# Optimization experiments

Hardware: AMD Instinct MI355X
Metric: run time of the kernel (lower is better)

The kernel has to match this reference:

```python
import jax, jax.numpy as jnp
import numpy as np

B = 8192       # atmospheric columns (batch)
NLAY = 60      # vertical levels (RNN sequence length)
NX = 4         # per-level input features
NXS = 3        # surface scalar inputs
NH1 = 64       # rnn1 hidden
NH2 = 64       # rnn2 hidden
NMEM = 16      # latent memory width (nh_mem)
NY = 4         # per-level outputs
NYS = 3        # surface outputs


def _lstm(x, h0, c0, Wih, Whh, bih, bhh):
    """PyTorch-convention LSTM (gate order i,f,g,o). x: [B,T,nx] -> ([B,T,nh], hL, cL)."""
    b = bih + bhh
    WihT = Wih.T
    WhhT = Whh.T

    def step(carry, xt):
        h, c = carry
        g = xt @ WihT + h @ WhhT + b
        i, f, gg, o = jnp.split(g, 4, axis=-1)
        c = jax.nn.sigmoid(f) * c + jax.nn.sigmoid(i) * jnp.tanh(gg)
        h = jax.nn.sigmoid(o) * jnp.tanh(c)
        return (h, c), h

    (hL, cL), ys = jax.lax.scan(step, (h0, c0), jnp.swapaxes(x, 0, 1))
    return jnp.swapaxes(ys, 0, 1), hL, cL


def setup_inputs() -> dict:
    key = jax.random.key(0)
    ks = jax.random.split(key, 30)

    def p(i, shape):
        return jax.random.normal(ks[i], shape, jnp.float32) * 0.05

    return {
        "inputs_main": jax.random.normal(ks[0], (B, NLAY, NX), jnp.float32),
        "inputs_aux": jax.random.normal(ks[1], (B, NXS), jnp.float32),
        "rnn1_mem": jax.random.normal(ks[2], (B, NLAY, NMEM), jnp.float32),
        # mlp_initial: Linear(nx, nneur[0])
        "Wi": p(3, (NH1, NX)), "bi": p(4, (NH1,)),
        # mlp_surface1/2: Linear(nx_sfc, nh_rnn1)
        "Ws1": p(5, (NH1, NXS)), "bs1": p(6, (NH1,)),
        "Ws2": p(7, (NH1, NXS)), "bs2": p(8, (NH1,)),
        # mlp_toa1/2: Linear(1, nh_rnn2)
        "Wt1": p(9, (NH2, 1)), "bt1": p(10, (NH2,)),
        "Wt2": p(11, (NH2, 1)), "bt2": p(12, (NH2,)),
        # rnn1: LSTM(NH1+NMEM -> NH1)
        "Wih1": p(13, (4 * NH1, NH1 + NMEM)), "Whh1": p(14, (4 * NH1, NH1)),
        "bih1": p(15, (4 * NH1,)), "bhh1": p(16, (4 * NH1,)),
        # rnn2: LSTM(NH1 -> NH2)
        "Wih2": p(17, (4 * NH2, NH1)), "Whh2": p(18, (4 * NH2, NH2)),
        "bih2": p(19, (4 * NH2,)), "bhh2": p(20, (4 * NH2,)),
        # mlp_latent: Linear(NH2, NMEM)
        "Wl": p(21, (NMEM, NH2)), "bl": p(22, (NMEM,)),
        # mlp_output: Linear(NMEM, NY)
        "Wo": p(23, (NY, NMEM)), "bo": p(24, (NY,)),
        # mlp_surface_output: Linear(NH2, NYS)
        "Wso": p(25, (NYS, NH2)), "bso": p(26, (NYS,)),
    }


def reference(inputs_main, inputs_aux, rnn1_mem, Wi, bi, Ws1, bs1, Ws2, bs2,
              Wt1, bt1, Wt2, bt2, Wih1, Whh1, bih1, bhh1, Wih2, Whh2, bih2, bhh2,
              Wl, bl, Wo, bo, Wso, bso):
    # initial MLP + tanh
    x = jnp.tanh(inputs_main @ Wi.T + bi)                       # [B,L,NH1]
    # concat convective memory
    x = jnp.concatenate([x, rnn1_mem], axis=2)                  # [B,L,NH1+NMEM]
    # rnn1 runs surface->TOA: flip level axis
    x = jnp.flip(x, axis=1)
    hx = jnp.tanh(inputs_aux @ Ws1.T + bs1)                     # surface-conditioned h0
    cx = jnp.tanh(inputs_aux @ Ws2.T + bs2)
    r1, _, _ = _lstm(x, hx, cx, Wih1, Whh1, bih1, bhh1)
    r1 = jnp.flip(r1, axis=1)                                   # back to TOA->surface
    # rnn2 initialized from TOA scalar
    toa = inputs_aux[:, 1:2]
    hx2 = toa @ Wt1.T + bt1
    cx2 = toa @ Wt2.T + bt2
    r2, hL, _ = _lstm(r1, hx2, cx2, Wih2, Whh2, bih2, bhh2)     # [B,L,NH2]
    # intermediate latent MLP -> new per-level memory
    lat = r2 @ Wl.T + bl                                        # [B,L,NMEM]
    new_mem = lat
    out = lat @ Wo.T + bo                                       # [B,L,NY]
    out_sfc = hL @ Wso.T + bso                                  # [B,NYS]
    return (out, out_sfc, new_mem)
```

## Files before the change

### kernel.cpp

```cpp
#include <hip/hip_runtime.h>
#include <hip/hip_bf16.h>

#define BATCH 8192
#define NLAY  60
#define ROWS  16
#define TPB   256
#define SX    136
#define SM    968
#define SI    244
#define LOG2E 1.44269504089f
#define T2L   2.88539008178f

typedef unsigned short ushort_t;
typedef __attribute__((ext_vector_type(8))) short short8;
typedef __attribute__((ext_vector_type(4))) float f32x4;
typedef __attribute__((ext_vector_type(4))) float f4v;

__device__ __forceinline__ float rcp_(float x) { return __builtin_amdgcn_rcpf(x); }
__device__ __forceinline__ float ex2_(float x) { return __builtin_amdgcn_exp2f(x); }
__device__ __forceinline__ ushort_t f2bu(float f) {
  unsigned u = __float_as_uint(f);
  return (ushort_t)((u + 0x7FFFu + ((u >> 16) & 1u)) >> 16);
}
__device__ __forceinline__ unsigned pkbf(float a, float b) {
  union { __hip_bfloat162 h; unsigned u; } c;
  c.h = __float22bfloat162_rn(make_float2(a, b));
  return c.u;
}
__device__ __forceinline__ f32x4 mfma16(short8 a, short8 b, f32x4 c) {
  return __builtin_amdgcn_mfma_f32_16x16x32_bf16(a, b, c, 0, 0, 0);
}
#define BAR() asm volatile("s_waitcnt lgkmcnt(0)\n\ts_barrier" ::: "memory")

__global__ void wtranspose(const float* __restrict__ Wih1, const float* __restrict__ Whh1,
                           const float* __restrict__ Wih2, const float* __restrict__ Whh2,
                           const float* __restrict__ Wl,   const float* __restrict__ Wo,
                           const float* __restrict__ Wso,  ushort_t* __restrict__ frag) {
  int e = blockIdx.x * 256 + threadIdx.x;
  float v;
  if (e < 40960) {
    int j = e & 7, lx = (e >> 3) & 63, rest = e >> 9;
    int ks = rest % 5, gw = rest / 5;
    int g = gw & 3, wv = gw >> 2;
    int row = g * 64 + wv * 16 + (lx & 15);
    int k = ks * 32 + (lx >> 4) * 8 + j;
    v = (k < 64)  ? Wih1[row * 80 + k]
      : (k < 128) ? Whh1[row * 64 + (k - 64)]
      : (k < 144) ? Wih1[row * 80 + 64 + (k - 128)]
      : 0.0f;
    v *= (g == 2) ? T2L : LOG2E;
  } else if (e < 73728) {
    int e2 = e - 40960;
    int j = e2 & 7, lx = (e2 >> 3) & 63, rest = e2 >> 9;
    int ks = rest & 3, g = (rest >> 2) & 3, wv = rest >> 4;
    int row = g * 64 + wv * 16 + (lx & 15);
    int k = ks * 32 + (lx >> 4) * 8 + j;
    v = (k < 64) ? Wih2[row * 64 + k] : Whh2[row * 64 + (k - 64)];
    v *= (g == 2) ? T2L : LOG2E;
  } else if (e < 74752) {
    int e3 = e - 73728;
    int j = e3 & 7, lx = (e3 >> 3) & 63, ks = e3 >> 9;
    int n = lx & 15, k = ks * 32 + (lx >> 4) * 8 + j;
    v = Wl[n * 64 + k];
  } else if (e < 75776) {
    int e4 = e - 74752;
    int j = e4 & 7, lx = (e4 >> 3) & 63, ks = e4 >> 9;
    int n = lx & 15, k = ks * 32 + (lx >> 4) * 8 + j;
    v = 0.0f;
    if (n < 4) {
#pragma unroll
      for (int m = 0; m < 16; ++m) v += Wo[n * 16 + m] * Wl[m * 64 + k];
    }
  } else {
    int e5 = e - 75776;
    int j = e5 & 7, lx = (e5 >> 3) & 63, ks = e5 >> 9;
    int n = lx & 15, k = ks * 32 + (lx >> 4) * 8 + j;
    v = (n < 3) ? Wso[n * 64 + k] : 0.0f;
  }
  frag[e] = f2bu(v);
}

__global__ __launch_bounds__(TPB, 2)
void lstm_fused(const float* __restrict__ inputs_main, const float* __restrict__ inputs_aux,
                const float* __restrict__ rnn1_mem,
                const float* __restrict__ Wi,  const float* __restrict__ bi,
                const float* __restrict__ Ws1, const float* __restrict__ bs1,
                const float* __restrict__ Ws2, const float* __restrict__ bs2,
                const float* __restrict__ Wt1, const float* __restrict__ bt1,
                const float* __restrict__ Wt2, const float* __restrict__ bt2,
                const float* __restrict__ bih1, const float* __restrict__ bhh1,
                const float* __restrict__ bih2, const float* __restrict__ bhh2,
                const float* __restrict__ bl,  const float* __restrict__ Wo,
                const float* __restrict__ bo,  const float* __restrict__ bso,
                const ushort_t* __restrict__ frag,
                ushort_t* __restrict__ r1buf,
                float* __restrict__ out, float* __restrict__ out_sfc,
                float* __restrict__ new_mem) {
  const ushort_t* W1f = frag;
  const ushort_t* W2f = frag + 40960;
  const ushort_t* WlF = frag + 73728;
  const ushort_t* WcF = frag + 74752;
  const ushort_t* WsF = frag + 75776;

  __shared__ __align__(16) ushort_t xh[2][16 * SX];
  __shared__ __align__(16) ushort_t memAll[16 * SM];
  __shared__ __align__(16) float    inm[16 * SI];

  const int tid = threadIdx.x;
  const int lane = tid & 63, w = tid >> 6;
  const int ln = lane & 15, lq = lane >> 4;
  const int u = w * 16 + ln;
  const int rowbase = lq * 4;
  const int b0 = blockIdx.x * ROWS;
  const int xr = tid >> 4, xm = tid & 15, xc0 = xm * 4;
  const int rr8 = tid >> 3, ch8 = tid & 7;

  ushort_t* r1blk = r1buf + (size_t)blockIdx.x * (60 * 16 * 64);

  short8 B1f[4][5];
#pragma unroll
  for (int g = 0; g < 4; ++g)
#pragma unroll
    for (int ks = 0; ks < 5; ++ks)
      B1f[g][ks] = *(const short8*)(W1f + (((w * 4 + g) * 5 + ks) << 9) + (lane << 3));
  float bg1[4];
#pragma unroll
  for (int g = 0; g < 4; ++g)
    bg1[g] = (bih1[g * 64 + u] + bhh1[g * 64 + u]) * ((g == 2) ? T2L : LOG2E);

  f4v wif[4];
#pragma unroll
  for (int cc = 0; cc < 4; ++cc) wif[cc] = *(const f4v*)(Wi + (xc0 + cc) * 4) * T2L;
  f4v bifv = *(const f4v*)(bi + xc0) * T2L;

  for (int e = tid; e < 16 * 240; e += TPB) {
    int r = e / 240, c = e - r * 240;
    inm[r * SI + c] = inputs_main[(size_t)(b0 + r) * 240 + c];
  }
  for (int e = tid; e < 16 * 960; e += TPB) {
    int r = e / 960, c = e - r * 960;
    memAll[r * SM + c] = f2bu(rnn1_mem[(size_t)(b0 + r) * 960 + c]);
  }
  __syncthreads();

  float ct1[4];
  {
    f4v xin = *(const f4v*)&inm[xr * SI + 59 * 4];
    float xp[4];
#pragma unroll
    for (int cc = 0; cc < 4; ++cc) {
      float a = fmaf(wif[cc][3], xin[3], fmaf(wif[cc][2], xin[2],
                fmaf(wif[cc][1], xin[1], fmaf(wif[cc][0], xin[0], bifv[cc]))));
      xp[cc] = fmaf(rcp_(1.0f + ex2_(a)), -2.0f, 1.0f);
    }
    *(uint2*)&xh[0][xr * SX + xc0] = make_uint2(pkbf(xp[0], xp[1]), pkbf(xp[2], xp[3]));

    float w10 = Ws1[u * 3 + 0] * T2L, w11 = Ws1[u * 3 + 1] * T2L, w12 = Ws1[u * 3 + 2] * T2L;
    float bb1 = bs1[u] * T2L;
    float w20 = Ws2[u * 3 + 0] * T2L, w21 = Ws2[u * 3 + 1] * T2L, w22 = Ws2[u * 3 + 2] * T2L;
    float bb2 = bs2[u] * T2L;
#pragma unroll
    for (int reg = 0; reg < 4; ++reg) {
      int row = rowbase + reg;
      const float* ax = inputs_aux + (size_t)(b0 + row) * 3;
      float a0 = ax[0], a1 = ax[1], a2 = ax[2];
      float ha = w10 * a0 + w11 * a1 + w12 * a2 + bb1;
      xh[0][row * SX + 64 + u] = f2bu(fmaf(rcp_(1.0f + ex2_(ha)), -2.0f, 1.0f));
      float ca = w20 * a0 + w21 * a1 + w22 * a2 + bb2;
      ct1[reg] = fmaf(rcp_(1.0f + ex2_(ca)), -2.0f * T2L, T2L);
    }
  }
  __syncthreads();

  ushort_t* r1t = r1blk + rowbase * 64 + u;
  unsigned sxv[4], syv[4];
  int pb = 0;

  for (int tg = 14; tg >= 0; --tg) {
#pragma unroll
    for (int s = 3; s >= 0; --s) {
      const int t = tg * 4 + s;
      const int nb = pb ^ 1;
      const ushort_t* xrow = &xh[pb][ln * SX];
      short8 af0 = *(const short8*)(xrow + lq * 8);
      short8 af1 = *(const short8*)(xrow + 32 + lq * 8);
      short8 af2 = *(const short8*)(xrow + 64 + lq * 8);
      short8 af3 = *(const short8*)(xrow + 96 + lq * 8);
      short8 af4 = {};
      if (lq < 2) af4 = *(const short8*)(memAll + ln * SM + t * 16 + lq * 8);

      f32x4 acc[4];
#pragma unroll
      for (int g = 0; g < 4; ++g) acc[g] = (f32x4){bg1[g], bg1[g], bg1[g], bg1[g]};
      __builtin_amdgcn_s_setprio(1);
#pragma unroll
      for (int g = 0; g < 4; ++g) {
        acc[g] = mfma16(af0, B1f[g][0], acc[g]);
        acc[g] = mfma16(af1, B1f[g][1], acc[g]);
        acc[g] = mfma16(af2, B1f[g][2], acc[g]);
        acc[g] = mfma16(af3, B1f[g][3], acc[g]);
        acc[g] = mfma16(af4, B1f[g][4], acc[g]);
      }
      __builtin_amdgcn_s_setprio(0);

      if (t > 0) {
        f4v xin = *(const f4v*)&inm[xr * SI + (t - 1) * 4];
        float xp[4];
#pragma unroll
        for (int cc = 0; cc < 4; ++cc) {
          float a = fmaf(wif[cc][3], xin[3], fmaf(wif[cc][2], xin[2],
                    fmaf(wif[cc][1], xin[1], fmaf(wif[cc][0], xin[0], bifv[cc]))));
          xp[cc] = fmaf(rcp_(1.0f + ex2_(a)), -2.0f, 1.0f);
        }
        *(uint2*)&xh[nb][xr * SX + xc0] = make_uint2(pkbf(xp[0], xp[1]), pkbf(xp[2], xp[3]));
      }

      float h[4];
#pragma unroll
      for (int reg = 0; reg < 4; ++reg) {
        float si = rcp_(1.0f + ex2_(-acc[0][reg]));
        float sf = rcp_(1.0f + ex2_(-acc[1][reg]));
        float so = rcp_(1.0f + ex2_(-acc[3][reg]));
        float gt = fmaf(rcp_(1.0f + ex2_(acc[2][reg])), -2.0f * T2L, T2L);
        ct1[reg] = fmaf(sf, ct1[reg], si * gt);
        float tc = fmaf(rcp_(1.0f + ex2_(ct1[reg])), -2.0f, 1.0f);
        h[reg] = so * tc;
      }
      unsigned h01 = pkbf(h[0], h[1]), h23 = pkbf(h[2], h[3]);
      sxv[s] = h01; syv[s] = h23;
      if (t > 0) {
        xh[nb][(rowbase + 0) * SX + 64 + u] = (ushort_t)h01;
        xh[nb][(rowbase + 1) * SX + 64 + u] = (ushort_t)(h01 >> 16);
        xh[nb][(rowbase + 2) * SX + 64 + u] = (ushort_t)h23;
        xh[nb][(rowbase + 3) * SX + 64 + u] = (ushort_t)(h23 >> 16);
      } else {
        xh[nb][(rowbase + 0) * SX + u] = (ushort_t)h01;
        xh[nb][(rowbase + 1) * SX + u] = (ushort_t)(h01 >> 16);
        xh[nb][(rowbase + 2) * SX + u] = (ushort_t)h23;
        xh[nb][(rowbase + 3) * SX + u] = (ushort_t)(h23 >> 16);
      }
      BAR();
      pb = nb;
    }
    ushort_t* rp = r1t + (tg << 12);
#pragma unroll
    for (int s = 0; s < 4; ++s) {
      unsigned a = sxv[s], b = syv[s];
      rp[s * 1024 + 0 * 64] = (ushort_t)a;
      rp[s * 1024 + 1 * 64] = (ushort_t)(a >> 16);
      rp[s * 1024 + 2 * 64] = (ushort_t)b;
      rp[s * 1024 + 3 * 64] = (ushort_t)(b >> 16);
    }
  }

  short8 B2f[4][4];
#pragma unroll
  for (int g = 0; g < 4; ++g)
#pragma unroll
    for (int ks = 0; ks < 4; ++ks)
      B2f[g][ks] = *(const short8*)(W2f + (((w * 4 + g) * 4 + ks) << 9) + (lane << 3));
  float bg2[4];
#pragma unroll
  for (int g = 0; g < 4; ++g)
    bg2[g] = (bih2[g * 64 + u] + bhh2[g * 64 + u]) * ((g == 2) ? T2L : LOG2E);

  float ct2[4];
  {
    float wt1u = Wt1[u], wt2u = Wt2[u], bt1u = bt1[u], bt2u = bt2[u];
#pragma unroll
    for (int reg = 0; reg < 4; ++reg) {
      int row = rowbase + reg;
      float toa = inputs_aux[(size_t)(b0 + row) * 3 + 1];
      xh[pb][row * SX + 64 + u] = f2bu(toa * wt1u + bt1u);
      ct2[reg] = (toa * wt2u + bt2u) * T2L;
    }
  }
  short8 PW0 = {}, PW1 = {};
  float pbias = 0.0f;
  if (w == 0) {
    PW0 = *(const short8*)(WlF + (lane << 3));
    PW1 = *(const short8*)(WlF + 512 + (lane << 3));
    pbias = bl[ln];
  } else if (w == 1) {
    PW0 = *(const short8*)(WcF + (lane << 3));
    PW1 = *(const short8*)(WcF + 512 + (lane << 3));
    if (ln < 4) {
      float a = bo[ln];
#pragma unroll
      for (int m = 0; m < 16; ++m) a += Wo[ln * 16 + m] * bl[m];
      pbias = a;
    }
  } else if (w == 2) {
    PW0 = *(const short8*)(WsF + (lane << 3));
    PW1 = *(const short8*)(WsF + 512 + (lane << 3));
    pbias = (ln < 3) ? bso[ln] : 0.0f;
  }
  const ushort_t* r1rp = r1blk + 1024 + rr8 * 64 + ch8 * 8;
  float* nmb = new_mem + (size_t)(b0 + rowbase) * 960 + ln;
  float* outb = out + (size_t)(b0 + rowbase) * 240 + ln;
  f32x4 pst[4];
  __syncthreads();

  for (int tg = 0; tg < 15; ++tg) {
#pragma unroll
    for (int s = 0; s < 4; ++s) {
      const int t = tg * 4 + s;
      const int nb = pb ^ 1;
      short8 r1v = {};
      if (t < 59 && tid < 128) r1v = *(const short8*)(r1rp + t * 1024);

      const ushort_t* xrow = &xh[pb][ln * SX];
      short8 af0 = *(const short8*)(xrow + lq * 8);
      short8 af1 = *(const short8*)(xrow + 32 + lq * 8);
      short8 af2 = *(const short8*)(xrow + 64 + lq * 8);
      short8 af3 = *(const short8*)(xrow + 96 + lq * 8);

      f32x4 acc[4];
#pragma unroll
      for (int g = 0; g < 4; ++g) acc[g] = (f32x4){bg2[g], bg2[g], bg2[g], bg2[g]};
      __builtin_amdgcn_s_setprio(1);
#pragma unroll
      for (int g = 0; g < 4; ++g) {
        acc[g] = mfma16(af0, B2f[g][0], acc[g]);
        acc[g] = mfma16(af1, B2f[g][1], acc[g]);
        acc[g] = mfma16(af2, B2f[g][2], acc[g]);
        acc[g] = mfma16(af3, B2f[g][3], acc[g]);
      }

      if (t > 0 && w < 2) {
        f32x4 ap = (f32x4){pbias, pbias, pbias, pbias};
        ap = mfma16(af2, PW0, ap);
        ap = mfma16(af3, PW1, ap);
        pst[(t - 1) & 3] = ap;
      }
      __builtin_amdgcn_s_setprio(0);

      float h[4];
#pragma unroll
      for (int reg = 0; reg < 4; ++reg) {
        float si = rcp_(1.0f + ex2_(-acc[0][reg]));
        float sf = rcp_(1.0f + ex2_(-acc[1][reg]));
        float so = rcp_(1.0f + ex2_(-acc[3][reg]));
        float gt = fmaf(rcp_(1.0f + ex2_(acc[2][reg])), -2.0f * T2L, T2L);
        ct2[reg] = fmaf(sf, ct2[reg], si * gt);
        float tc = fmaf(rcp_(1.0f + ex2_(ct2[reg])), -2.0f, 1.0f);
        h[reg] = so * tc;
      }
      unsigned h01 = pkbf(h[0], h[1]), h23 = pkbf(h[2], h[3]);
      xh[nb][(rowbase + 0) * SX + 64 + u] = (ushort_t)h01;
      xh[nb][(rowbase + 1) * SX + 64 + u] = (ushort_t)(h01 >> 16);
      xh[nb][(rowbase + 2) * SX + 64 + u] = (ushort_t)h23;
      xh[nb][(rowbase + 3) * SX + 64 + u] = (ushort_t)(h23 >> 16);
      if (t < 59 && tid < 128)
        *(short8*)&xh[nb][rr8 * SX + ch8 * 8] = r1v;
      BAR();
      pb = nb;
    }
    if (w < 2) {
      const int base = tg * 4;
#pragma unroll
      for (int k = 0; k < 4; ++k) {
        const int pt = (k == 3) ? base - 1 : base + k;
        if (pt < 0) continue;
        f32x4 ap = pst[k];
        if (w == 0) {
#pragma unroll
          for (int reg = 0; reg < 4; ++reg) nmb[reg * 960 + pt * 16] = ap[reg];
        } else if (ln < 4) {
#pragma unroll
          for (int reg = 0; reg < 4; ++reg) outb[reg * 240 + pt * 4] = ap[reg];
        }
      }
    }
  }

  if (w < 3) {
    const ushort_t* xrow = &xh[pb][ln * SX];
    short8 aL0 = *(const short8*)(xrow + 64 + lq * 8);
    short8 aL1 = *(const short8*)(xrow + 96 + lq * 8);
    f32x4 ap = (f32x4){pbias, pbias, pbias, pbias};
    ap = mfma16(aL0, PW0, ap);
    ap = mfma16(aL1, PW1, ap);
    if (w == 0) {
#pragma unroll
      for (int reg = 0; reg < 4; ++reg) nmb[reg * 960 + 59 * 16] = ap[reg];
    } else if (w == 1) {
      if (ln < 4) {
#pragma unroll
        for (int reg = 0; reg < 4; ++reg) outb[reg * 240 + 59 * 4] = ap[reg];
      }
    } else {
      if (ln < 3) {
#pragma unroll
        for (int reg = 0; reg < 4; ++reg)
          out_sfc[(size_t)(b0 + rowbase + reg) * 3 + ln] = ap[reg];
      }
    }
  }
}

extern "C" void kernel_launch(void* const* d_in, const int* in_sizes, int n_in,
                              void* d_out, int out_size, void* d_ws, size_t ws_size,
                              hipStream_t stream) {
  (void)in_sizes; (void)n_in; (void)out_size; (void)ws_size;
  const float* inputs_main = (const float*)d_in[0];
  const float* inputs_aux  = (const float*)d_in[1];
  const float* rnn1_mem    = (const float*)d_in[2];
  const float* Wi   = (const float*)d_in[3];
  const float* bi   = (const float*)d_in[4];
  const float* Ws1  = (const float*)d_in[5];
  const float* bs1  = (const float*)d_in[6];
  const float* Ws2  = (const float*)d_in[7];
  const float* bs2  = (const float*)d_in[8];
  const float* Wt1  = (const float*)d_in[9];
  const float* bt1  = (const float*)d_in[10];
  const float* Wt2  = (const float*)d_in[11];
  const float* bt2  = (const float*)d_in[12];
  const float* Wih1 = (const float*)d_in[13];
  const float* Whh1 = (const float*)d_in[14];
  const float* bih1 = (const float*)d_in[15];
  const float* bhh1 = (const float*)d_in[16];
  const float* Wih2 = (const float*)d_in[17];
  const float* Whh2 = (const float*)d_in[18];
  const float* bih2 = (const float*)d_in[19];
  const float* bhh2 = (const float*)d_in[20];
  const float* Wl   = (const float*)d_in[21];
  const float* bl   = (const float*)d_in[22];
  const float* Wo   = (const float*)d_in[23];
  const float* bo   = (const float*)d_in[24];
  const float* Wso  = (const float*)d_in[25];
  const float* bso  = (const float*)d_in[26];

  float* out     = (float*)d_out;
  float* out_sfc = out + (size_t)BATCH * NLAY * 4;
  float* new_mem = out_sfc + (size_t)BATCH * 3;

  ushort_t* frag  = (ushort_t*)d_ws;
  ushort_t* r1buf = (ushort_t*)((char*)d_ws + 153600);

  wtranspose<<<300, 256, 0, stream>>>(Wih1, Whh1, Wih2, Whh2, Wl, Wo, Wso, frag);
  lstm_fused<<<BATCH / ROWS, TPB, 0, stream>>>(
      inputs_main, inputs_aux, rnn1_mem, Wi, bi, Ws1, bs1, Ws2, bs2,
      Wt1, bt1, Wt2, bt2, bih1, bhh1, bih2, bhh2, bl, Wo, bo, bso,
      frag, r1buf, out, out_sfc, new_mem);
}
```

Before: 253.9 us.

## Process two 16-row groups per block to interleave independent LSTM recurrences

Each block now handles 32 batch rows as two independent 16-row groups, issuing both groups' MFMA chains and gate math in each timestep. Two independent dependency chains per wave are meant to hide MFMA and transcendental latency within the serial recurrence, and one barrier now covers both groups. In exchange the grid halves to 256 blocks, launch bounds drop to one block per SIMD set, and LDS and register use roughly double. That cuts the number of resident waves and may leave some CUs idle.

Result: slower. 293.4 us (+15.5%).

```diff
diff --git a/kernel.cpp b/kernel.cpp
--- a/kernel.cpp
+++ b/kernel.cpp
@@ -3,7 +3,7 @@
 
 #define BATCH 8192
 #define NLAY  60
-#define ROWS  16
+#define ROWS  32
 #define TPB   256
 #define SX    136
 #define SM    968
@@ -80,7 +80,7 @@
   frag[e] = f2bu(v);
 }
 
-__global__ __launch_bounds__(TPB, 2)
+__global__ __launch_bounds__(TPB, 1)
 void lstm_fused(const float* __restrict__ inputs_main, const float* __restrict__ inputs_aux,
                 const float* __restrict__ rnn1_mem,
                 const float* __restrict__ Wi,  const float* __restrict__ bi,
@@ -102,9 +102,9 @@
   const ushort_t* WcF = frag + 74752;
   const ushort_t* WsF = frag + 75776;
 
-  __shared__ __align__(16) ushort_t xh[2][16 * SX];
-  __shared__ __align__(16) ushort_t memAll[16 * SM];
-  __shared__ __align__(16) float    inm[16 * SI];
+  __shared__ __align__(16) ushort_t xh[2][2][16 * SX];
+  __shared__ __align__(16) ushort_t memAll[2][16 * SM];
+  __shared__ __align__(16) float    inm[2][16 * SI];
 
   const int tid = threadIdx.x;
   const int lane = tid & 63, w = tid >> 6;
@@ -112,10 +112,11 @@
   const int u = w * 16 + ln;
   const int rowbase = lq * 4;
   const int b0 = blockIdx.x * ROWS;
-  const int xr = tid >> 4, xm = tid & 15, xc0 = xm * 4;
-  const int rr8 = tid >> 3, ch8 = tid & 7;
-
-  ushort_t* r1blk = r1buf + (size_t)blockIdx.x * (60 * 16 * 64);
+  const int xr = tid >> 4, xc0 = (tid & 15) * 4;
+  const int gsel = tid >> 7, tl = tid & 127;
+  const int rr8 = tl >> 3, ch8 = tl & 7;
+
+  ushort_t* r1blk = r1buf + (size_t)blockIdx.x * (60 * 32 * 64);
 
   short8 B1f[4][5];
 #pragma unroll
@@ -133,47 +134,50 @@
   for (int cc = 0; cc < 4; ++cc) wif[cc] = *(const f4v*)(Wi + (xc0 + cc) * 4) * T2L;
   f4v bifv = *(const f4v*)(bi + xc0) * T2L;
 
-  for (int e = tid; e < 16 * 240; e += TPB) {
+  for (int e = tid; e < 32 * 240; e += TPB) {
     int r = e / 240, c = e - r * 240;
-    inm[r * SI + c] = inputs_main[(size_t)(b0 + r) * 240 + c];
-  }
-  for (int e = tid; e < 16 * 960; e += TPB) {
+    inm[r >> 4][(r & 15) * SI + c] = inputs_main[(size_t)(b0 + r) * 240 + c];
+  }
+  for (int e = tid; e < 32 * 960; e += TPB) {
     int r = e / 960, c = e - r * 960;
-    memAll[r * SM + c] = f2bu(rnn1_mem[(size_t)(b0 + r) * 960 + c]);
+    memAll[r >> 4][(r & 15) * SM + c] = f2bu(rnn1_mem[(size_t)(b0 + r) * 960 + c]);
   }
   __syncthreads();
 
-  float ct1[4];
+  float ct1[2][4];
   {
-    f4v xin = *(const f4v*)&inm[xr * SI + 59 * 4];
-    float xp[4];
-#pragma unroll
-    for (int cc = 0; cc < 4; ++cc) {
-      float a = fmaf(wif[cc][3], xin[3], fmaf(wif[cc][2], xin[2],
-                fmaf(wif[cc][1], xin[1], fmaf(wif[cc][0], xin[0], bifv[cc]))));
-      xp[cc] = fmaf(rcp_(1.0f + ex2_(a)), -2.0f, 1.0f);
-    }
-    *(uint2*)&xh[0][xr * SX + xc0] = make_uint2(pkbf(xp[0], xp[1]), pkbf(xp[2], xp[3]));
-
+#pragma unroll
+    for (int G = 0; G < 2; ++G) {
+      f4v xin = *(const f4v*)&inm[G][xr * SI + 59 * 4];
+      float xp[4];
+#pragma unroll
+      for (int cc = 0; cc < 4; ++cc) {
+        float a = fmaf(wif[cc][3], xin[3], fmaf(wif[cc][2], xin[2],
+                  fmaf(wif[cc][1], xin[1], fmaf(wif[cc][0], xin[0], bifv[cc]))));
+        xp[cc] = fmaf(rcp_(1.0f + ex2_(a)), -2.0f, 1.0f);
+      }
+      *(uint2*)&xh[G][0][xr * SX + xc0] = make_uint2(pkbf(xp[0], xp[1]), pkbf(xp[2], xp[3]));
+    }
     float w10 = Ws1[u * 3 + 0] * T2L, w11 = Ws1[u * 3 + 1] * T2L, w12 = Ws1[u * 3 + 2] * T2L;
     float bb1 = bs1[u] * T2L;
     float w20 = Ws2[u * 3 + 0] * T2L, w21 = Ws2[u * 3 + 1] * T2L, w22 = Ws2[u * 3 + 2] * T2L;
     float bb2 = bs2[u] * T2L;
 #pragma unroll
-    for (int reg = 0; reg < 4; ++reg) {
-      int row = rowbase + reg;
-      const float* ax = inputs_aux + (size_t)(b0 + row) * 3;
-      float a0 = ax[0], a1 = ax[1], a2 = ax[2];
-      float ha = w10 * a0 + w11 * a1 + w12 * a2 + bb1;
-      xh[0][row * SX + 64 + u] = f2bu(fmaf(rcp_(1.0f + ex2_(ha)), -2.0f, 1.0f));
-      float ca = w20 * a0 + w21 * a1 + w22 * a2 + bb2;
-      ct1[reg] = fmaf(rcp_(1.0f + ex2_(ca)), -2.0f * T2L, T2L);
-    }
+    for (int G = 0; G < 2; ++G)
+#pragma unroll
+      for (int reg = 0; reg < 4; ++reg) {
+        int row = rowbase + reg;
+        const float* ax = inputs_aux + (size_t)(b0 + G * 16 + row) * 3;
+        float a0 = ax[0], a1 = ax[1], a2 = ax[2];
+        float ha = w10 * a0 + w11 * a1 + w12 * a2 + bb1;
+        xh[G][0][row * SX + 64 + u] = f2bu(fmaf(rcp_(1.0f + ex2_(ha)), -2.0f, 1.0f));
+        float ca = w20 * a0 + w21 * a1 + w22 * a2 + bb2;
+        ct1[G][reg] = fmaf(rcp_(1.0f + ex2_(ca)), -2.0f * T2L, T2L);
+      }
   }
   __syncthreads();
 
-  ushort_t* r1t = r1blk + rowbase * 64 + u;
-  unsigned sxv[4], syv[4];
+  unsigned sxv[2][4], syv[2][4];
   int pb = 0;
 
   for (int tg = 14; tg >= 0; --tg) {
@@ -181,75 +185,93 @@
     for (int s = 3; s >= 0; --s) {
       const int t = tg * 4 + s;
       const int nb = pb ^ 1;
-      const ushort_t* xrow = &xh[pb][ln * SX];
-      short8 af0 = *(const short8*)(xrow + lq * 8);
-      short8 af1 = *(const short8*)(xrow + 32 + lq * 8);
-      short8 af2 = *(const short8*)(xrow + 64 + lq * 8);
-      short8 af3 = *(const short8*)(xrow + 96 + lq * 8);
-      short8 af4 = {};
-      if (lq < 2) af4 = *(const short8*)(memAll + ln * SM + t * 16 + lq * 8);
-
-      f32x4 acc[4];
-#pragma unroll
-      for (int g = 0; g < 4; ++g) acc[g] = (f32x4){bg1[g], bg1[g], bg1[g], bg1[g]};
+      short8 af[2][5];
+#pragma unroll
+      for (int G = 0; G < 2; ++G) {
+        const ushort_t* xrow = &xh[G][pb][ln * SX];
+        af[G][0] = *(const short8*)(xrow + lq * 8);
+        af[G][1] = *(const short8*)(xrow + 32 + lq * 8);
+        af[G][2] = *(const short8*)(xrow + 64 + lq * 8);
+        af[G][3] = *(const short8*)(xrow + 96 + lq * 8);
+        af[G][4] = (short8){};
+        if (lq < 2) af[G][4] = *(const short8*)(memAll[G] + ln * SM + t * 16 + lq * 8);
+      }
+
+      f32x4 acc[2][4];
+#pragma unroll
+      for (int G = 0; G < 2; ++G)
+#pragma unroll
+        for (int g = 0; g < 4; ++g) acc[G][g] = (f32x4){bg1[g], bg1[g], bg1[g], bg1[g]};
       __builtin_amdgcn_s_setprio(1);
 #pragma unroll
-      for (int g = 0; g < 4; ++g) {
-        acc[g] = mfma16(af0, B1f[g][0], acc[g]);
-        acc[g] = mfma16(af1, B1f[g][1], acc[g]);
-        acc[g] = mfma16(af2, B1f[g][2], acc[g]);
-        acc[g] = mfma16(af3, B1f[g][3], acc[g]);
-        acc[g] = mfma16(af4, B1f[g][4], acc[g]);
-      }
+      for (int g = 0; g < 4; ++g)
+#pragma unroll
+        for (int G = 0; G < 2; ++G) {
+          acc[G][g] = mfma16(af[G][0], B1f[g][0], acc[G][g]);
+          acc[G][g] = mfma16(af[G][1], B1f[g][1], acc[G][g]);
+          acc[G][g] = mfma16(af[G][2], B1f[g][2], acc[G][g]);
+          acc[G][g] = mfma16(af[G][3], B1f[g][3], acc[G][g]);
+          acc[G][g] = mfma16(af[G][4], B1f[g][4], acc[G][g]);
+        }
       __builtin_amdgcn_s_setprio(0);
 
       if (t > 0) {
-        f4v xin = *(const f4v*)&inm[xr * SI + (t - 1) * 4];
-        float xp[4];
-#pragma unroll
-        for (int cc = 0; cc < 4; ++cc) {
-          float a = fmaf(wif[cc][3], xin[3], fmaf(wif[cc][2], xin[2],
-                    fmaf(wif[cc][1], xin[1], fmaf(wif[cc][0], xin[0], bifv[cc]))));
-          xp[cc] = fmaf(rcp_(1.0f + ex2_(a)), -2.0f, 1.0f);
-        }
-        *(uint2*)&xh[nb][xr * SX + xc0] = make_uint2(pkbf(xp[0], xp[1]), pkbf(xp[2], xp[3]));
-      }
-
-      float h[4];
-#pragma unroll
-      for (int reg = 0; reg < 4; ++reg) {
-        float si = rcp_(1.0f + ex2_(-acc[0][reg]));
-        float sf = rcp_(1.0f + ex2_(-acc[1][reg]));
-        float so = rcp_(1.0f + ex2_(-acc[3][reg]));
-        float gt = fmaf(rcp_(1.0f + ex2_(acc[2][reg])), -2.0f * T2L, T2L);
-        ct1[reg] = fmaf(sf, ct1[reg], si * gt);
-        float tc = fmaf(rcp_(1.0f + ex2_(ct1[reg])), -2.0f, 1.0f);
-        h[reg] = so * tc;
-      }
-      unsigned h01 = pkbf(h[0], h[1]), h23 = pkbf(h[2], h[3]);
-      sxv[s] = h01; syv[s] = h23;
-      if (t > 0) {
-        xh[nb][(rowbase + 0) * SX + 64 + u] = (ushort_t)h01;
-        xh[nb][(rowbase + 1) * SX + 64 + u] = (ushort_t)(h01 >> 16);
-        xh[nb][(rowbase + 2) * SX + 64 + u] = (ushort_t)h23;
-        xh[nb][(rowbase + 3) * SX + 64 + u] = (ushort_t)(h23 >> 16);
-      } else {
-        xh[nb][(rowbase + 0) * SX + u] = (ushort_t)h01;
-        xh[nb][(rowbase + 1) * SX + u] = (ushort_t)(h01 >> 16);
-        xh[nb][(rowbase + 2) * SX + u] = (ushort_t)h23;
-        xh[nb][(rowbase + 3) * SX + u] = (ushort_t)(h23 >> 16);
+#pragma unroll
+        for (int G = 0; G < 2; ++G) {
+          f4v xin = *(const f4v*)&inm[G][xr * SI + (t - 1) * 4];
+          float xp[4];
+#pragma unroll
+          for (int cc = 0; cc < 4; ++cc) {
+            float a = fmaf(wif[cc][3], xin[3], fmaf(wif[cc][2], xin[2],
+                      fmaf(wif[cc][1], xin[1], fmaf(wif[cc][0], xin[0], bifv[cc]))));
+            xp[cc] = fmaf(rcp_(1.0f + ex2_(a)), -2.0f, 1.0f);
+          }
+          *(uint2*)&xh[G][nb][xr * SX + xc0] =
+              make_uint2(pkbf(xp[0], xp[1]), pkbf(xp[2], xp[3]));
+        }
+      }
+
+#pragma unroll
+      for (int G = 0; G < 2; ++G) {
+        float h[4];
+#pragma unroll
+        for (int reg = 0; reg < 4; ++reg) {
+          float si = rcp_(1.0f + ex2_(-acc[G][0][reg]));
+          float sf = rcp_(1.0f + ex2_(-acc[G][1][reg]));
+          float so = rcp_(1.0f + ex2_(-acc[G][3][reg]));
+          float gt = fmaf(rcp_(1.0f + ex2_(acc[G][2][reg])), -2.0f * T2L, T2L);
+          ct1[G][reg] = fmaf(sf, ct1[G][reg], si * gt);
+          float tc = fmaf(rcp_(1.0f + ex2_(ct1[G][reg])), -2.0f, 1.0f);
+          h[reg] = so * tc;
+        }
+        unsigned h01 = pkbf(h[0], h[1]), h23 = pkbf(h[2], h[3]);
+        sxv[G][s] = h01; syv[G][s] = h23;
+        if (t > 0) {
+          xh[G][nb][(rowbase + 0) * SX + 64 + u] = (ushort_t)h01;
+          xh[G][nb][(rowbase + 1) * SX + 64 + u] = (ushort_t)(h01 >> 16);
+          xh[G][nb][(rowbase + 2) * SX + 64 + u] = (ushort_t)h23;
+          xh[G][nb][(rowbase + 3) * SX + 64 + u] = (ushort_t)(h23 >> 16);
+        } else {
+          xh[G][nb][(rowbase + 0) * SX + u] = (ushort_t)h01;
+          xh[G][nb][(rowbase + 1) * SX + u] = (ushort_t)(h01 >> 16);
+          xh[G][nb][(rowbase + 2) * SX + u] = (ushort_t)h23;
+          xh[G][nb][(rowbase + 3) * SX + u] = (ushort_t)(h23 >> 16);
+        }
       }
       BAR();
       pb = nb;
     }
-    ushort_t* rp = r1t + (tg << 12);
-#pragma unroll
-    for (int s = 0; s < 4; ++s) {
-      unsigned a = sxv[s], b = syv[s];
-      rp[s * 1024 + 0 * 64] = (ushort_t)a;
-      rp[s * 1024 + 1 * 64] = (ushort_t)(a >> 16);
-      rp[s * 1024 + 2 * 64] = (ushort_t)b;
-      rp[s * 1024 + 3 * 64] = (ushort_t)(b >> 16);
+#pragma unroll
+    for (int G = 0; G < 2; ++G) {
+      ushort_t* rp = r1blk + G * 61440 + (tg << 12) + rowbase * 64 + u;
+#pragma unroll
+      for (int s = 0; s < 4; ++s) {
+        unsigned a = sxv[G][s], b = syv[G][s];
+        rp[s * 1024 + 0 * 64] = (ushort_t)a;
+        rp[s * 1024 + 1 * 64] = (ushort_t)(a >> 16);
+        rp[s * 1024 + 2 * 64] = (ushort_t)b;
+        rp[s * 1024 + 3 * 64] = (ushort_t)(b >> 16);
+      }
     }
   }
 
@@ -264,16 +286,18 @@
   for (int g = 0; g < 4; ++g)
     bg2[g] = (bih2[g * 64 + u] + bhh2[g * 64 + u]) * ((g == 2) ? T2L : LOG2E);
 
-  float ct2[4];
+  float ct2[2][4];
   {
     float wt1u = Wt1[u], wt2u = Wt2[u], bt1u = bt1[u], bt2u = bt2[u];
 #pragma unroll
-    for (int reg = 0; reg < 4; ++reg) {
-      int row = rowbase + reg;
-      float toa = inputs_aux[(size_t)(b0 + row) * 3 + 1];
-      xh[pb][row * SX + 64 + u] = f2bu(toa * wt1u + bt1u);
-      ct2[reg] = (toa * wt2u + bt2u) * T2L;
-    }
+    for (int G = 0; G < 2; ++G)
+#pragma unroll
+      for (int reg = 0; reg < 4; ++reg) {
+        int row = rowbase + reg;
+        float toa = inputs_aux[(size_t)(b0 + G * 16 + row) * 3 + 1];
+        xh[G][pb][row * SX + 64 + u] = f2bu(toa * wt1u + bt1u);
+        ct2[G][reg] = (toa * wt2u + bt2u) * T2L;
+      }
   }
   short8 PW0 = {}, PW1 = {};
   float pbias = 0.0f;
@@ -295,10 +319,14 @@
     PW1 = *(const short8*)(WsF + 512 + (lane << 3));
     pbias = (ln < 3) ? bso[ln] : 0.0f;
   }
-  const ushort_t* r1rp = r1blk + 1024 + rr8 * 64 + ch8 * 8;
-  float* nmb = new_mem + (size_t)(b0 + rowbase) * 960 + ln;
-  float* outb = out + (size_t)(b0 + rowbase) * 240 + ln;
-  f32x4 pst[4];
+  const ushort_t* r1rp = r1blk + gsel * 61440 + 1024 + rr8 * 64 + ch8 * 8;
+  float* nmb[2];  float* outb[2];
+#pragma unroll
+  for (int G = 0; G < 2; ++G) {
+    nmb[G]  = new_mem + (size_t)(b0 + G * 16 + rowbase) * 960 + ln;
+    outb[G] = out + (size_t)(b0 + G * 16 + rowbase) * 240 + ln;
+  }
+  f32x4 pst[2][4];
   __syncthreads();
 
   for (int tg = 0; tg < 15; ++tg) {
@@ -307,93 +335,110 @@
       const int t = tg * 4 + s;
       const int nb = pb ^ 1;
       short8 r1v = {};
-      if (t < 59 && tid < 128) r1v = *(const short8*)(r1rp + t * 1024);
-
-      const ushort_t* xrow = &xh[pb][ln * SX];
-      short8 af0 = *(const short8*)(xrow + lq * 8);
-      short8 af1 = *(const short8*)(xrow + 32 + lq * 8);
-      short8 af2 = *(const short8*)(xrow + 64 + lq * 8);
-      short8 af3 = *(const short8*)(xrow + 96 + lq * 8);
-
-      f32x4 acc[4];
-#pragma unroll
-      for (int g = 0; g < 4; ++g) acc[g] = (f32x4){bg2[g], bg2[g], bg2[g], bg2[g]};
+      if (t < 59) r1v = *(const short8*)(r1rp + t * 1024);
+
+      short8 af[2][4];
+#pragma unroll
+      for (int G = 0; G < 2; ++G) {
+        const ushort_t* xrow = &xh[G][pb][ln * SX];
+        af[G][0] = *(const short8*)(xrow + lq * 8);
+        af[G][1] = *(const short8*)(xrow + 32 + lq * 8);
+        af[G][2] = *(const short8*)(xrow + 64 + lq * 8);
+        af[G][3] = *(const short8*)(xrow + 96 + lq * 8);
+      }
+
+      f32x4 acc[2][4];
+#pragma unroll
+      for (int G = 0; G < 2; ++G)
+#pragma unroll
+        for (int g = 0; g < 4; ++g) acc[G][g] = (f32x4){bg2[g], bg2[g], bg2[g], bg2[g]};
       __builtin_amdgcn_s_setprio(1);
 #pragma unroll
-      for (int g = 0; g < 4; ++g) {
-        acc[g] = mfma16(af0, B2f[g][0], acc[g]);
-        acc[g] = mfma16(af1, B2f[g][1], acc[g]);
-        acc[g] = mfma16(af2, B2f[g][2], acc[g]);
-        acc[g] = mfma16(af3, B2f[g][3], acc[g]);
-      }
-
+      for (int g = 0; g < 4; ++g)
+#pragma unroll
+        for (int G = 0; G < 2; ++G) {
+          acc[G][g] = mfma16(af[G][0], B2f[g][0], acc[G][g]);
+          acc[G][g] = mfma16(af[G][1], B2f[g][1], acc[G][g]);
+          acc[G][g] = mfma16(af[G][2], B2f[g][2], acc[G][g]);
+          acc[G][g] = mfma16(af[G][3], B2f[g][3], acc[G][g]);
+        }
       if (t > 0 && w < 2) {
-        f32x4 ap = (f32x4){pbias, pbias, pbias, pbias};
-        ap = mfma16(af2, PW0, ap);
-        ap = mfma16(af3, PW1, ap);
-        pst[(t - 1) & 3] = ap;
+#pragma unroll
+        for (int G = 0; G < 2; ++G) {
+          f32x4 ap = (f32x4){pbias, pbias, pbias, pbias};
+          ap = mfma16(af[G][2], PW0, ap);
+          ap = mfma16(af[G][3], PW1, ap);
+          pst[G][(t - 1) & 3] = ap;
+        }
       }
       __builtin_amdgcn_s_setprio(0);
 
-      float h[4];
-#pragma unroll
-      for (int reg = 0; reg < 4; ++reg) {
-        float si = rcp_(1.0f + ex2_(-acc[0][reg]));
-        float sf = rcp_(1.0f + ex2_(-acc[1][reg]));
-        float so = rcp_(1.0f + ex2_(-acc[3][reg]));
-        float gt = fmaf(rcp_(1.0f + ex2_(acc[2][reg])), -2.0f * T2L, T2L);
-        ct2[reg] = fmaf(sf, ct2[reg], si * gt);
-        float tc = fmaf(rcp_(1.0f + ex2_(ct2[reg])), -2.0f, 1.0f);
-        h[reg] = so * tc;
-      }
-      unsigned h01 = pkbf(h[0], h[1]), h23 = pkbf(h[2], h[3]);
-      xh[nb][(rowbase + 0) * SX + 64 + u] = (ushort_t)h01;
-      xh[nb][(rowbase + 1) * SX + 64 + u] = (ushort_t)(h01 >> 16);
-      xh[nb][(rowbase + 2) * SX + 64 + u] = (ushort_t)h23;
-      xh[nb][(rowbase + 3) * SX + 64 + u] = (ushort_t)(h23 >> 16);
-      if (t < 59 && tid < 128)
-        *(short8*)&xh[nb][rr8 * SX + ch8 * 8] = r1v;
+#pragma unroll
+      for (int G = 0; G < 2; ++G) {
+        float h[4];
+#pragma unroll
+        for (int reg = 0; reg < 4; ++reg) {
+          float si = rcp_(1.0f + ex2_(-acc[G][0][reg]));
+          float sf = rcp_(1.0f + ex2_(-acc[G][1][reg]));
+          float so = rcp_(1.0f + ex2_(-acc[G][3][reg]));
+          float gt = fmaf(rcp_(1.0f + ex2_(acc[G][2][reg])), -2.0f * T2L, T2L);
+          ct2[G][reg] = fmaf(sf, ct2[G][reg], si * gt);
+          float tc = fmaf(rcp_(1.0f + ex2_(ct2[G][reg])), -2.0f, 1.0f);
+          h[reg] = so * tc;
+        }
+        unsigned h01 = pkbf(h[0], h[1]), h23 = pkbf(h[2], h[3]);
+        xh[G][nb][(rowbase + 0) * SX + 64 + u] = (ushort_t)h01;
+        xh[G][nb][(rowbase + 1) * SX + 64 + u] = (ushort_t)(h01 >> 16);
+        xh[G][nb][(rowbase + 2) * SX + 64 + u] = (ushort_t)h23;
+        xh[G][nb][(rowbase + 3) * SX + 64 + u] = (ushort_t)(h23 >> 16);
+      }
+      if (t < 59) *(short8*)&xh[gsel][nb][rr8 * SX + ch8 * 8] = r1v;
       BAR();
       pb = nb;
     }
     if (w < 2) {
       const int base = tg * 4;
 #pragma unroll
-      for (int k = 0; k < 4; ++k) {
-        const int pt = (k == 3) ? base - 1 : base + k;
-        if (pt < 0) continue;
-        f32x4 ap = pst[k];
-        if (w == 0) {
-#pragma unroll
-          for (int reg = 0; reg < 4; ++reg) nmb[reg * 960 + pt * 16] = ap[reg];
-        } else if (ln < 4) {
-#pragma unroll
-          for (int reg = 0; reg < 4; ++reg) outb[reg * 240 + pt * 4] = ap[reg];
-        }
-      }
+      for (int G = 0; G < 2; ++G)
+#pragma unroll
+        for (int k = 0; k < 4; ++k) {
+          const int pt = (k == 3) ? base - 1 : base + k;
+          if (pt < 0) continue;
+          f32x4 ap = pst[G][k];
+          if (w == 0) {
+#pragma unroll
+            for (int reg = 0; reg < 4; ++reg) nmb[G][reg * 960 + pt * 16] = ap[reg];
+          } else if (ln < 4) {
+#pragma unroll
+            for (int reg = 0; reg < 4; ++reg) outb[G][reg * 240 + pt * 4] = ap[reg];
+          }
+        }
     }
   }
 
   if (w < 3) {
-    const ushort_t* xrow = &xh[pb][ln * SX];
-    short8 aL0 = *(const short8*)(xrow + 64 + lq * 8);
-    short8 aL1 = *(const short8*)(xrow + 96 + lq * 8);
-    f32x4 ap = (f32x4){pbias, pbias, pbias, pbias};
-    ap = mfma16(aL0, PW0, ap);
-    ap = mfma16(aL1, PW1, ap);
-    if (w == 0) {
-#pragma unroll
-      for (int reg = 0; reg < 4; ++reg) nmb[reg * 960 + 59 * 16] = ap[reg];
-    } else if (w == 1) {
-      if (ln < 4) {
-#pragma unroll
-        for (int reg = 0; reg < 4; ++reg) outb[reg * 240 + 59 * 4] = ap[reg];
-      }
-    } else {
-      if (ln < 3) {
-#pragma unroll
-        for (int reg = 0; reg < 4; ++reg)
-          out_sfc[(size_t)(b0 + rowbase + reg) * 3 + ln] = ap[reg];
+#pragma unroll
+    for (int G = 0; G < 2; ++G) {
+      const ushort_t* xrow = &xh[G][pb][ln * SX];
+      short8 aL0 = *(const short8*)(xrow + 64 + lq * 8);
+      short8 aL1 = *(const short8*)(xrow + 96 + lq * 8);
+      f32x4 ap = (f32x4){pbias, pbias, pbias, pbias};
+      ap = mfma16(aL0, PW0, ap);
+      ap = mfma16(aL1, PW1, ap);
+      if (w == 0) {
+#pragma unroll
+        for (int reg = 0; reg < 4; ++reg) nmb[G][reg * 960 + 59 * 16] = ap[reg];
+      } else if (w == 1) {
+        if (ln < 4) {
+#pragma unroll
+          for (int reg = 0; reg < 4; ++reg) outb[G][reg * 240 + 59 * 4] = ap[reg];
+        }
+      } else {
+        if (ln < 3) {
+#pragma unroll
+          for (int reg = 0; reg < 4; ++reg)
+            out_sfc[(size_t)(b0 + G * 16 + rowbase + reg) * 3 + ln] = ap[reg];
+        }
       }
     }
   }
```

## Precompute initial MLP in separate kernel and stream inputs through r1 buffer

Applied to the files above, without the earlier changes.

Moves the initial tanh(Wi x + bi) projection into a new xgen kernel that writes bf16 results into the r1buf workspace. Inside the recurrent loop, each step now loads the precomputed x slice from global memory rather than computing it with exp/rcp, and the r1 outputs overwrite the same buffer slots in place. The inm shared buffer is dropped and the rnn1_mem staging is vectorised. This trades per-step transcendental ALU work on the serial critical path for an extra kernel launch, extra global traffic, and a global load per step.

New measurement: 289.5 us. +14.0%, slower.

```diff
diff --git a/kernel.cpp b/kernel.cpp
--- a/kernel.cpp
+++ b/kernel.cpp
@@ -7,7 +7,6 @@
 #define TPB   256
 #define SX    136
 #define SM    968
-#define SI    244
 #define LOG2E 1.44269504089f
 #define T2L   2.88539008178f
 
@@ -80,10 +79,28 @@
   frag[e] = f2bu(v);
 }
 
+__global__ void xgen(const float* __restrict__ inputs_main, const float* __restrict__ Wi,
+                     const float* __restrict__ bi, ushort_t* __restrict__ r1buf) {
+  int id = blockIdx.x * 256 + threadIdx.x;
+  int b = id / 960, rem = id - b * 960;
+  int t = rem >> 4, q = rem & 15;
+  f4v xin = *(const f4v*)(inputs_main + (size_t)b * 240 + t * 4);
+  float xp[4];
+#pragma unroll
+  for (int cc = 0; cc < 4; ++cc) {
+    int ch = q * 4 + cc;
+    f4v wv = *(const f4v*)(Wi + ch * 4);
+    float a = (wv[0] * xin[0] + wv[1] * xin[1] + wv[2] * xin[2] + wv[3] * xin[3]
+               + bi[ch]) * T2L;
+    xp[cc] = fmaf(rcp_(1.0f + ex2_(a)), -2.0f, 1.0f);
+  }
+  ushort_t* dst = r1buf + (size_t)(b >> 4) * 61440 + t * 1024 + (b & 15) * 64 + q * 4;
+  *(uint2*)dst = make_uint2(pkbf(xp[0], xp[1]), pkbf(xp[2], xp[3]));
+}
+
 __global__ __launch_bounds__(TPB, 2)
-void lstm_fused(const float* __restrict__ inputs_main, const float* __restrict__ inputs_aux,
+void lstm_fused(const float* __restrict__ inputs_aux,
                 const float* __restrict__ rnn1_mem,
-                const float* __restrict__ Wi,  const float* __restrict__ bi,
                 const float* __restrict__ Ws1, const float* __restrict__ bs1,
                 const float* __restrict__ Ws2, const float* __restrict__ bs2,
                 const float* __restrict__ Wt1, const float* __restrict__ bt1,
@@ -104,7 +121,6 @@
 
   __shared__ __align__(16) ushort_t xh[2][16 * SX];
   __shared__ __align__(16) ushort_t memAll[16 * SM];
-  __shared__ __align__(16) float    inm[16 * SI];
 
   const int tid = threadIdx.x;
   const int lane = tid & 63, w = tid >> 6;
@@ -112,7 +128,6 @@
   const int u = w * 16 + ln;
   const int rowbase = lq * 4;
   const int b0 = blockIdx.x * ROWS;
-  const int xr = tid >> 4, xm = tid & 15, xc0 = xm * 4;
   const int rr8 = tid >> 3, ch8 = tid & 7;
 
   ushort_t* r1blk = r1buf + (size_t)blockIdx.x * (60 * 16 * 64);
@@ -128,33 +143,18 @@
   for (int g = 0; g < 4; ++g)
     bg1[g] = (bih1[g * 64 + u] + bhh1[g * 64 + u]) * ((g == 2) ? T2L : LOG2E);
 
-  f4v wif[4];
-#pragma unroll
-  for (int cc = 0; cc < 4; ++cc) wif[cc] = *(const f4v*)(Wi + (xc0 + cc) * 4) * T2L;
-  f4v bifv = *(const f4v*)(bi + xc0) * T2L;
-
   for (int e = tid; e < 16 * 240; e += TPB) {
     int r = e / 240, c = e - r * 240;
-    inm[r * SI + c] = inputs_main[(size_t)(b0 + r) * 240 + c];
-  }
-  for (int e = tid; e < 16 * 960; e += TPB) {
-    int r = e / 960, c = e - r * 960;
-    memAll[r * SM + c] = f2bu(rnn1_mem[(size_t)(b0 + r) * 960 + c]);
-  }
-  __syncthreads();
+    f4v mv = *(const f4v*)(rnn1_mem + (size_t)(b0 + r) * 960 + c * 4);
+    *(uint2*)&memAll[r * SM + c * 4] = make_uint2(pkbf(mv[0], mv[1]), pkbf(mv[2], mv[3]));
+  }
+  if (tid < 128) {
+    short8 xv = *(const short8*)(r1blk + 59 * 1024 + rr8 * 64 + ch8 * 8);
+    *(short8*)&xh[0][rr8 * SX + ch8 * 8] = xv;
+  }
 
   float ct1[4];
   {
-    f4v xin = *(const f4v*)&inm[xr * SI + 59 * 4];
-    float xp[4];
-#pragma unroll
-    for (int cc = 0; cc < 4; ++cc) {
-      float a = fmaf(wif[cc][3], xin[3], fmaf(wif[cc][2], xin[2],
-                fmaf(wif[cc][1], xin[1], fmaf(wif[cc][0], xin[0], bifv[cc]))));
-      xp[cc] = fmaf(rcp_(1.0f + ex2_(a)), -2.0f, 1.0f);
-    }
-    *(uint2*)&xh[0][xr * SX + xc0] = make_uint2(pkbf(xp[0], xp[1]), pkbf(xp[2], xp[3]));
-
     float w10 = Ws1[u * 3 + 0] * T2L, w11 = Ws1[u * 3 + 1] * T2L, w12 = Ws1[u * 3 + 2] * T2L;
     float bb1 = bs1[u] * T2L;
     float w20 = Ws2[u * 3 + 0] * T2L, w21 = Ws2[u * 3 + 1] * T2L, w22 = Ws2[u * 3 + 2] * T2L;
@@ -181,6 +181,10 @@
     for (int s = 3; s >= 0; --s) {
       const int t = tg * 4 + s;
       const int nb = pb ^ 1;
+      short8 xv;
+      const bool lx = (t > 0) && (tid < 128);
+      if (lx) xv = *(const short8*)(r1blk + (size_t)(t - 1) * 1024 + rr8 * 64 + ch8 * 8);
+
       const ushort_t* xrow = &xh[pb][ln * SX];
       short8 af0 = *(const short8*)(xrow + lq * 8);
       short8 af1 = *(const short8*)(xrow + 32 + lq * 8);
@@ -202,18 +206,6 @@
         acc[g] = mfma16(af4, B1f[g][4], acc[g]);
       }
       __builtin_amdgcn_s_setprio(0);
-
-      if (t > 0) {
-        f4v xin = *(const f4v*)&inm[xr * SI + (t - 1) * 4];
-        float xp[4];
-#pragma unroll
-        for (int cc = 0; cc < 4; ++cc) {
-          float a = fmaf(wif[cc][3], xin[3], fmaf(wif[cc][2], xin[2],
-                    fmaf(wif[cc][1], xin[1], fmaf(wif[cc][0], xin[0], bifv[cc]))));
-          xp[cc] = fmaf(rcp_(1.0f + ex2_(a)), -2.0f, 1.0f);
-        }
-        *(uint2*)&xh[nb][xr * SX + xc0] = make_uint2(pkbf(xp[0], xp[1]), pkbf(xp[2], xp[3]));
-      }
 
       float h[4];
 #pragma unroll
@@ -239,6 +231,7 @@
         xh[nb][(rowbase + 2) * SX + u] = (ushort_t)h23;
         xh[nb][(rowbase + 3) * SX + u] = (ushort_t)(h23 >> 16);
       }
+      if (lx) *(short8*)&xh[nb][rr8 * SX + ch8 * 8] = xv;
       BAR();
       pb = nb;
     }
@@ -439,8 +432,9 @@
   ushort_t* r1buf = (ushort_t*)((char*)d_ws + 153600);
 
   wtranspose<<<300, 256, 0, stream>>>(Wih1, Whh1, Wih2, Whh2, Wl, Wo, Wso, frag);
+  xgen<<<BATCH * NLAY * 16 / TPB, TPB, 0, stream>>>(inputs_main, Wi, bi, r1buf);
   lstm_fused<<<BATCH / ROWS, TPB, 0, stream>>>(
-      inputs_main, inputs_aux, rnn1_mem, Wi, bi, Ws1, bs1, Ws2, bs2,
+      inputs_aux, rnn1_mem, Ws1, bs1, Ws2, bs2,
       Wt1, bt1, Wt2, bt2, bih1, bhh1, bih2, bhh2, bl, Wo, bo, bso,
       frag, r1buf, out, out_sfc, new_mem);
 }
```
